# Performance work log

Measured on AMD Instinct MI355X. Metric: run time of the kernel, lower is better.

Reference implementation:

```python
import jax, jax.numpy as jnp
import numpy as np

S, B, I, H, MLP, K = 1024, 64, 512, 256, 512, 64  # seq_len, batch, input, hidden, mlp, n_sections


def setup_inputs() -> dict:
    key = jax.random.key(0)
    ks = jax.random.split(key, 12)
    inputs = jax.random.normal(ks[0], (S, B, I), jnp.float32)
    input_length = jnp.full((B,), S, dtype=jnp.int32)  # full-length seqs -> pack/pad is identity
    # contiguous section boundaries per document; indices address pad_output of length S+1
    bounds = jnp.sort(jax.random.randint(ks[1], (B, K + 1), 0, S + 1), axis=1)
    begin = bounds[:, :-1].astype(jnp.int32)
    end = bounds[:, 1:].astype(jnp.int32)
    # one-hot section membership per token: [B, S, K]
    sec = jax.random.randint(ks[2], (B, S), 0, K)
    section_indicator = jax.nn.one_hot(sec, K, dtype=jnp.float32)
    s = 1.0 / np.sqrt(H)
    u = lambda k, shape: jax.random.uniform(k, shape, jnp.float32, -s, s)
    params = {
        'W_ih_f': u(ks[3], (3 * H, I)), 'W_hh_f': u(ks[4], (3 * H, H)),
        'b_ih_f': u(ks[5], (3 * H,)), 'b_hh_f': u(ks[5], (3 * H,)),
        'W_ih_b': u(ks[6], (3 * H, I)), 'W_hh_b': u(ks[7], (3 * H, H)),
        'b_ih_b': u(ks[8], (3 * H,)), 'b_hh_b': u(ks[8], (3 * H,)),
        'W1': u(ks[9], (MLP, 4 * H)), 'b1': u(ks[9], (MLP,)),
        'W2': u(ks[10], (1, MLP)), 'b2': u(ks[10], (1,)),
    }
    return dict(inputs=inputs, input_length=input_length,
                section_indicator=section_indicator, begin=begin, end=end, **params)


def _gru_dir(x, Wi, Wh, bi, bh, reverse):
    """One direction of a torch-style GRU. x: [S,B,I] -> hiddens [S,B,H]."""
    xi = jnp.einsum('sbi,gi->sbg', x, Wi) + bi  # precompute input projections [S,B,3H]
    Bsz = x.shape[1]
    Hn = Wh.shape[1]

    def step(h, xt):
        gh = h @ Wh.T + bh
        xr, xz, xn = jnp.split(xt, 3, axis=-1)
        hr, hz, hn = jnp.split(gh, 3, axis=-1)
        r = jax.nn.sigmoid(xr + hr)
        z = jax.nn.sigmoid(xz + hz)
        n = jnp.tanh(xn + r * hn)
        hnew = (1.0 - z) * n + z * h
        return hnew, hnew

    h0 = jnp.zeros((Bsz, Hn), x.dtype)
    _, hs = jax.lax.scan(step, h0, xi, reverse=reverse)
    return hs


def reference(inputs, input_length, section_indicator, begin, end,
              W_ih_f, W_hh_f, b_ih_f, b_hh_f,
              W_ih_b, W_hh_b, b_ih_b, b_hh_b,
              W1, b1, W2, b2):
    # bi-GRU (dropout layers are identity in eval mode)
    out_f = _gru_dir(inputs, W_ih_f, W_hh_f, b_ih_f, b_hh_f, reverse=False)
    out_b = _gru_dir(inputs, W_ih_b, W_hh_b, b_ih_b, b_hh_b, reverse=True)
    output = jnp.concatenate([out_f, out_b], axis=-1)  # [S,B,2H]
    # prepend zero row along time: pad_output [S+1,B,2H]
    pad_output = jnp.concatenate([jnp.zeros((1,) + output.shape[1:], output.dtype), output], axis=0)
    po = jnp.transpose(pad_output, (1, 0, 2))  # [B,S+1,2H]
    g_end = jnp.take_along_axis(po, end[:, :, None], axis=1)    # [B,K,2H]
    g_beg = jnp.take_along_axis(po, begin[:, :, None], axis=1)  # [B,K,2H]
    Hn = output.shape[-1] // 2
    local = jnp.concatenate([g_end[..., :Hn] - g_beg[..., :Hn],
                             g_beg[..., Hn:] - g_end[..., Hn:]], axis=-1)  # [B,K,2H]
    lcr = jnp.einsum('bsk,bkd->bsd', section_indicator, local)  # [B,S,2H]
    lcr = jnp.transpose(lcr, (1, 0, 2))  # [S,B,2H]
    mlp_in = jnp.concatenate([output, lcr], axis=-1)  # [S,B,4H]
    h1 = jax.nn.relu(mlp_in @ W1.T + b1)
    out = h1 @ W2.T + b2  # [S,B,1]
    return out
```

## Files before the change

### kernel.cpp

```cpp
#include <hip/hip_runtime.h>

typedef unsigned short u16;
typedef __attribute__((ext_vector_type(2))) unsigned short u16x2;
typedef __attribute__((ext_vector_type(8))) short short8;
typedef __attribute__((ext_vector_type(4))) float f32x4;
typedef __attribute__((ext_vector_type(4))) int i32x4;

#define T_CHUNK 128
#define XI_DIRSZ ((size_t)T_CHUNK * 49152)

__device__ __forceinline__ u16 f2bf(float f) {
  unsigned u = __float_as_uint(f);
  u += 0x7FFFu + ((u >> 16) & 1u);
  return (u16)(u >> 16);
}
__device__ __forceinline__ float bf2f(u16 v) { return __uint_as_float(((unsigned)v) << 16); }
__device__ __forceinline__ short8 cvt8(const float* __restrict__ p) {
  float4 a = ((const float4*)p)[0];
  float4 b = ((const float4*)p)[1];
  short8 r;
  r[0] = (short)f2bf(a.x); r[1] = (short)f2bf(a.y); r[2] = (short)f2bf(a.z); r[3] = (short)f2bf(a.w);
  r[4] = (short)f2bf(b.x); r[5] = (short)f2bf(b.y); r[6] = (short)f2bf(b.z); r[7] = (short)f2bf(b.w);
  return r;
}

__global__ __launch_bounds__(256) void k_diag(float* o, float v) {
  if (threadIdx.x == 0 && blockIdx.x == 0) o[0] = v;
}

__global__ __launch_bounds__(256) void k_cvt(const float* __restrict__ s, u16* __restrict__ d, int n) {
  int i = blockIdx.x * 256 + threadIdx.x;
  int st = gridDim.x * 256;
  for (; i < n; i += st) d[i] = f2bf(s[i]);
}

__global__ __launch_bounds__(64) void k_quantw(const float* __restrict__ Wf, const float* __restrict__ Wb,
                                               signed char* __restrict__ Wq, float* __restrict__ rscale) {
  const int row = blockIdx.x;
  const int l = threadIdx.x;
  const float* src = (row < 768) ? (Wf + (size_t)row * 256) : (Wb + (size_t)(row - 768) * 256);
  float4 v = ((const float4*)src)[l];
  float m = fmaxf(fmaxf(fabsf(v.x), fabsf(v.y)), fmaxf(fabsf(v.z), fabsf(v.w)));
#pragma unroll
  for (int off = 32; off; off >>= 1) m = fmaxf(m, __shfl_xor(m, off));
  const float s = 127.f / m;
  char4 q;
  q.x = (signed char)(int)__builtin_rintf(v.x * s);
  q.y = (signed char)(int)__builtin_rintf(v.y * s);
  q.z = (signed char)(int)__builtin_rintf(v.z * s);
  q.w = (signed char)(int)__builtin_rintf(v.w * s);
  ((char4*)(Wq + (size_t)row * 256))[l] = q;
  if (l == 0) rscale[row] = m / (127.f * 127.f);
}

__device__ __forceinline__ int swz8b(int row, int off) {
  return row * 256 + ((((off >> 4) ^ (row * 5)) & 15) << 4) + (off & 15);
}

__device__ __forceinline__ void proj_body(int pid, int cn, const float* __restrict__ x,
                                          const u16* __restrict__ WihB, const float* __restrict__ bihf,
                                          const float* __restrict__ bihb, u16* __restrict__ xi,
                                          u16* Al, u16* Bl) {
  const int tid = threadIdx.x;
  const int l = tid & 63, w = tid >> 6;
  const int lm = l & 15, lq = l >> 4;
  const int dir = pid >= 1536;
  const int q = dir ? pid - 1536 : pid;
  const int r8 = q & 7, rest = q >> 3;
  const int bx = rest % 12;
  const int by = (rest / 12) * 8 + r8;
  const float* A = x + ((size_t)(dir ? (1024 - (cn + 1) * T_CHUNK) : (cn * T_CHUNK)) + by) * 32768;
  const u16* Bw = WihB + (size_t)dir * 393216;
  const float* bias = dir ? bihb : bihf;
  u16* xo = xi + ((size_t)((cn & 1) * 2 + dir)) * XI_DIRSZ;

  const int n0 = bx << 6;
  const int r0 = tid >> 3, c0 = (tid & 7) << 3;
  const int mt = w >> 1, nh = w & 1;
  f32x4 acc[2] = {};
  for (int k0 = 0; k0 < 512; k0 += 64) {
    __syncthreads();
    *(short8*)&Al[r0 * 72 + c0] = cvt8(A + (size_t)r0 * 512 + k0 + c0);
    *(short8*)&Bl[r0 * 72 + c0] = *(const short8*)(Bw + (size_t)(n0 + r0) * 512 + k0 + c0);
    __syncthreads();
#pragma unroll
    for (int kk = 0; kk < 2; ++kk) {
      short8 af = *(const short8*)&Al[(mt * 16 + lm) * 72 + kk * 32 + lq * 8];
#pragma unroll
      for (int ntp = 0; ntp < 2; ++ntp) {
        short8 bf = *(const short8*)&Bl[((nh * 2 + ntp) * 16 + lm) * 72 + kk * 32 + lq * 8];
        acc[ntp] = __builtin_amdgcn_mfma_f32_16x16x32_bf16(af, bf, acc[ntp], 0, 0, 0);
      }
    }
  }
#pragma unroll
  for (int ntp = 0; ntp < 2; ++ntp) {
    int n = n0 + (nh * 2 + ntp) * 16 + lm;
    float bv = bias[n];
#pragma unroll
    for (int r = 0; r < 4; ++r) {
      int b = mt * 16 + lq * 4 + r;
      xo[(((size_t)by * 8 + (b >> 3)) * 768 + n) * 8 + (b & 7)] = f2bf(acc[ntp][r] + bv);
    }
  }
}

__global__ __launch_bounds__(512, 2) void k_proj0(const float* __restrict__ x, const u16* __restrict__ WihB,
                                                  const float* __restrict__ bihf, const float* __restrict__ bihb,
                                                  u16* __restrict__ xi) {
  __shared__ __align__(16) u16 Al[64 * 72];
  __shared__ __align__(16) u16 Bl[64 * 72];
  proj_body(blockIdx.x, 0, x, WihB, bihf, bihb, xi, Al, Bl);
}

__global__ __launch_bounds__(512, 1) void k_fused(
    const float* __restrict__ x, const u16* __restrict__ WihB,
    const float* __restrict__ bihf, const float* __restrict__ bihb,
    u16* __restrict__ xi, const signed char* __restrict__ Wq, const float* __restrict__ rscale,
    const float* __restrict__ bhhf, const float* __restrict__ bhhb,
    float* __restrict__ carry, u16* __restrict__ ob, int chunk, int nscan) {
  __shared__ __align__(16) signed char hb8[2][1024];
  __shared__ __align__(16) u16 Al[64 * 72];
  __shared__ __align__(16) u16 Bl[64 * 72];

  const int tid = threadIdx.x;
  const int l = tid & 63, w = tid >> 6;
  const int lm = l & 15, lq = l >> 4;

  if ((int)blockIdx.x >= nscan) {
    proj_body(blockIdx.x - nscan, chunk + 1, x, WihB, bihf, bihb, xi, Al, Bl);
    return;
  }

  __builtin_amdgcn_s_setprio(1);
  const int dir = blockIdx.x >> 4;
  const int grp = blockIdx.x & 15;
  const int jhL = lq >> 1;
  const int b0 = (lq & 1) << 1;
  const int jL = w * 32 + jhL * 16 + lm;
  const int arow = lm & 3;
  const float* bhh = dir ? bhhb : bhhf;
  const u16* xic = xi + ((size_t)((chunk & 1) * 2 + dir)) * XI_DIRSZ;

  i32x4 bw[6][4];
#pragma unroll
  for (int g = 0; g < 3; ++g)
#pragma unroll
    for (int jh = 0; jh < 2; ++jh) {
      const int row = dir * 768 + g * 256 + w * 32 + jh * 16 + lm;
      const signed char* rp = Wq + (size_t)row * 256 + lq * 16;
#pragma unroll
      for (int kk = 0; kk < 4; ++kk) bw[g * 2 + jh][kk] = *(const i32x4*)(rp + kk * 64);
    }
  float rs[3];
#pragma unroll
  for (int g = 0; g < 3; ++g) rs[g] = rscale[dir * 768 + g * 256 + jL];
  const float bR = bhh[jL], bZ = bhh[256 + jL], bN = bhh[512 + jL];

  signed char* hbb = &hb8[0][0];
  float hreg[2];
  if (chunk == 0) {
    hreg[0] = 0.f; hreg[1] = 0.f;
    if (tid < 512) ((unsigned*)hbb)[tid] = 0;
  } else {
#pragma unroll
    for (int i = 0; i < 2; ++i) {
      float v = carry[(size_t)(dir * 64 + grp * 4 + b0 + i) * 256 + jL];
      hreg[i] = v;
      hbb[swz8b(b0 + i, jL)] = (signed char)(int)__builtin_rintf(fminf(fmaxf(v, -1.f), 1.f) * 127.f);
    }
  }

  const int stL0 = dir ? (T_CHUNK - 1) : 0;
  const u16* p_xi = xic + ((size_t)stL0 * 8 + (grp >> 1)) * 6144 + (size_t)jL * 8 + (grp & 1) * 4 + b0;
  const int tg0 = dir ? (1023 - chunk * T_CHUNK) : (chunk * T_CHUNK);
  u16* p_ob = ob + ((size_t)(tg0 * 64 + grp * 4 + b0)) * 512 + dir * 256 + jL;
  const ptrdiff_t dxi = dir ? -49152 : 49152;
  const ptrdiff_t dob = dir ? -32768 : 32768;
  __syncthreads();

  u16x2 xv[3];
#pragma unroll
  for (int g = 0; g < 3; ++g) xv[g] = *(const u16x2*)(p_xi + g * 2048);

  for (int st = 0; st < T_CHUNK; ++st) {
    const int cur = st & 1;
    const signed char* hcur = hbb + cur * 1024;
    i32x4 a4[4];
#pragma unroll
    for (int kk = 0; kk < 4; ++kk) a4[kk] = *(const i32x4*)(hcur + swz8b(arow, kk * 64 + lq * 16));
    p_xi += dxi;
    u16x2 xn[3];
    if (st < T_CHUNK - 1) {
#pragma unroll
      for (int g = 0; g < 3; ++g) xn[g] = *(const u16x2*)(p_xi + g * 2048);
    }

    i32x4 acc[2][3] = {};
#pragma unroll
    for (int kk = 0; kk < 4; ++kk)
#pragma unroll
      for (int jh = 0; jh < 2; ++jh)
#pragma unroll
        for (int g = 0; g < 3; ++g)
          acc[jh][g] = __builtin_amdgcn_mfma_i32_16x16x64_i8(a4[kk], bw[g * 2 + jh][kk], acc[jh][g], 0, 0, 0);

    signed char* hnxt = hbb + (cur ^ 1) * 1024;
    i32x4 accS[3];
#pragma unroll
    for (int g = 0; g < 3; ++g) accS[g] = (lq >= 2) ? acc[1][g] : acc[0][g];
#pragma unroll
    for (int i = 0; i < 2; ++i) {
      float fr = (float)((lq & 1) ? accS[0][2 + i] : accS[0][i]) * rs[0];
      float fz = (float)((lq & 1) ? accS[1][2 + i] : accS[1][i]) * rs[1];
      float fn = (float)((lq & 1) ? accS[2][2 + i] : accS[2][i]) * rs[2];
      float ar = bf2f(xv[0][i]) + fr + bR;
      float az = bf2f(xv[1][i]) + fz + bZ;
      float rr = __builtin_amdgcn_rcpf(1.f + __expf(-ar));
      float zz = __builtin_amdgcn_rcpf(1.f + __expf(-az));
      float an = bf2f(xv[2][i]) + rr * (fn + bN);
      float nn = 2.f * __builtin_amdgcn_rcpf(1.f + __expf(-2.f * an)) - 1.f;
      float hv = nn + zz * (hreg[i] - nn);
      hreg[i] = hv;
      hnxt[swz8b(b0 + i, jL)] = (signed char)(int)__builtin_rintf(fminf(fmaxf(hv, -1.f), 1.f) * 127.f);
      p_ob[(size_t)i * 512] = f2bf(hv);
    }
#pragma unroll
    for (int g = 0; g < 3; ++g) xv[g] = xn[g];
    p_ob += dob;
    asm volatile("s_waitcnt lgkmcnt(0)\n\ts_barrier" ::: "memory");
  }
  __builtin_amdgcn_s_setprio(0);
#pragma unroll
  for (int i = 0; i < 2; ++i)
    carry[(size_t)(dir * 64 + grp * 4 + b0 + i) * 256 + jL] = hreg[i];
}

__global__ __launch_bounds__(256) void k_local(const u16* __restrict__ ob, const int* __restrict__ bg,
                                               const int* __restrict__ en, u16* __restrict__ loc) {
  const int b = blockIdx.y, k = blockIdx.x, j = threadIdx.x;
  const int e = en[b * 64 + k], g = bg[b * 64 + k];
  const float ef  = e ? bf2f(ob[(size_t)((e - 1) * 64 + b) * 512 + j]) : 0.f;
  const float bf_ = g ? bf2f(ob[(size_t)((g - 1) * 64 + b) * 512 + j]) : 0.f;
  const float eb  = e ? bf2f(ob[(size_t)((e - 1) * 64 + b) * 512 + 256 + j]) : 0.f;
  const float bb_ = g ? bf2f(ob[(size_t)((g - 1) * 64 + b) * 512 + 256 + j]) : 0.f;
  const size_t o = ((size_t)b * 64 + k) * 512;
  loc[o + j] = f2bf(ef - bf_);
  loc[o + 256 + j] = f2bf(bb_ - eb);
}

__global__ __launch_bounds__(256) void k_sec(const float* __restrict__ ind, int* __restrict__ sec) {
  const int idx = blockIdx.x * 256 + threadIdx.x;
  const int s = idx >> 6, b = idx & 63;
  const float* row = ind + ((size_t)b * 1024 + s) * 64;
  int kk = 0;
  for (int q = 0; q < 64; ++q)
    if (row[q] > 0.5f) kk = q;
  sec[idx] = kk;
}

__global__ __launch_bounds__(256) void k_gemm_mlp(const u16* __restrict__ obb, const u16* __restrict__ locb,
                                                  const int* __restrict__ sec, const u16* __restrict__ W1b,
                                                  const float* __restrict__ b1, const float* __restrict__ W2,
                                                  float* __restrict__ partial) {
  __shared__ __align__(16) u16 Bl[128][64];
  const int tid = threadIdx.x;
  const int l = tid & 63, w = tid >> 6;
  const int lm = l & 15, lq = l >> 4;
  const int bid = blockIdx.x;
  const int mb = (bid >> 5) * 8 + (bid & 7);
  const int nh = (bid >> 3) & 3;
  const int m0 = mb << 7, n0 = nh << 7;

  const u16* pa[2];
  const u16* la[2];
#pragma unroll
  for (int mt = 0; mt < 2; ++mt) {
    int mA = m0 + w * 32 + mt * 16 + lm;
    pa[mt] = obb + (size_t)mA * 512;
    la[mt] = locb + ((size_t)(mA & 63) * 64 + sec[mA]) * 512 - 512;
  }
  const int br = tid >> 1;
  const int bh = tid & 1;
  const u16* wrow = W1b + (size_t)(n0 + br) * 1024 + bh * 32;

  short8 rb[4];
#pragma unroll
  for (int c = 0; c < 4; ++c) rb[c] = *(const short8*)(wrow + c * 8);
  short8 rA[2][2];
#pragma unroll
  for (int mt = 0; mt < 2; ++mt)
#pragma unroll
    for (int kk = 0; kk < 2; ++kk) rA[mt][kk] = *(const short8*)(pa[mt] + kk * 32 + lq * 8);

  f32x4 acc[2][8] = {};
  for (int k0 = 0; k0 < 1024; k0 += 64) {
    __syncthreads();
#pragma unroll
    for (int c = 0; c < 4; ++c)
      *(short8*)&Bl[br][(((bh * 4 + c) ^ (br & 7)) << 3)] = rb[c];
    __syncthreads();
    short8 aCur[2][2];
#pragma unroll
    for (int mt = 0; mt < 2; ++mt)
#pragma unroll
      for (int kk = 0; kk < 2; ++kk) aCur[mt][kk] = rA[mt][kk];
    if (k0 < 960) {
      const int kn = k0 + 64;
#pragma unroll
      for (int c = 0; c < 4; ++c) rb[c] = *(const short8*)(wrow + kn + c * 8);
#pragma unroll
      for (int mt = 0; mt < 2; ++mt) {
        const u16* base = (kn < 512) ? pa[mt] : la[mt];
#pragma unroll
        for (int kk = 0; kk < 2; ++kk) rA[mt][kk] = *(const short8*)(base + kn + kk * 32 + lq * 8);
      }
    }
#pragma unroll
    for (int kk = 0; kk < 2; ++kk)
#pragma unroll
      for (int nt = 0; nt < 8; ++nt) {
        const int rrow = nt * 16 + lm;
        short8 bf = *(const short8*)&Bl[rrow][(((kk * 4 + lq) ^ (rrow & 7)) << 3)];
#pragma unroll
        for (int mt = 0; mt < 2; ++mt)
          acc[mt][nt] = __builtin_amdgcn_mfma_f32_16x16x32_bf16(aCur[mt][kk], bf, acc[mt][nt], 0, 0, 0);
      }
  }
  float s[2][4];
#pragma unroll
  for (int mt = 0; mt < 2; ++mt)
#pragma unroll
    for (int r = 0; r < 4; ++r) s[mt][r] = 0.f;
#pragma unroll
  for (int nt = 0; nt < 8; ++nt) {
    int n = n0 + nt * 16 + lm;
    float bb = b1[n], ww = W2[n];
#pragma unroll
    for (int mt = 0; mt < 2; ++mt)
#pragma unroll
      for (int r = 0; r < 4; ++r) s[mt][r] += fmaxf(acc[mt][nt][r] + bb, 0.f) * ww;
  }
#pragma unroll
  for (int off = 1; off < 16; off <<= 1)
#pragma unroll
    for (int mt = 0; mt < 2; ++mt)
#pragma unroll
      for (int r = 0; r < 4; ++r) s[mt][r] += __shfl_xor(s[mt][r], off);
  if (lm == 0) {
#pragma unroll
    for (int mt = 0; mt < 2; ++mt)
#pragma unroll
      for (int r = 0; r < 4; ++r)
        partial[(size_t)nh * 65536 + m0 + w * 32 + mt * 16 + lq * 4 + r] = s[mt][r];
  }
}

__global__ __launch_bounds__(256) void k_fin2(const float* __restrict__ partial, const float* __restrict__ b2,
                                              float* __restrict__ o) {
  const int i = blockIdx.x * 256 + threadIdx.x;
  float s = b2[0];
#pragma unroll
  for (int q = 0; q < 4; ++q) s += partial[(size_t)q * 65536 + i];
  o[i] = s;
}

extern "C" void kernel_launch(void* const* d_in, const int* in_sizes, int n_in,
                              void* d_out, int out_size, void* d_ws, size_t ws_size,
                              hipStream_t stream) {
  (void)in_sizes; (void)n_in; (void)out_size;
  const float* x    = (const float*)d_in[0];
  const float* sind = (const float*)d_in[2];
  const int*   beg  = (const int*)d_in[3];
  const int*   endi = (const int*)d_in[4];
  const float* Wihf = (const float*)d_in[5];
  const float* Whhf = (const float*)d_in[6];
  const float* bihf = (const float*)d_in[7];
  const float* bhhf = (const float*)d_in[8];
  const float* Wihb = (const float*)d_in[9];
  const float* Whhb = (const float*)d_in[10];
  const float* bihb = (const float*)d_in[11];
  const float* bhhb = (const float*)d_in[12];
  const float* W1   = (const float*)d_in[13];
  const float* b1   = (const float*)d_in[14];
  const float* W2   = (const float*)d_in[15];
  const float* b2   = (const float*)d_in[16];

  const size_t NEED = 124911616ull;
  if (ws_size < NEED) {
    k_diag<<<dim3(1), dim3(256), 0, stream>>>((float*)d_out, 1000.f + (float)(ws_size >> 20));
    return;
  }

  char* ws = (char*)d_ws;
  u16*   xibuf = (u16*)(ws);
  u16*   obb   = (u16*)(ws + 50331648);
  u16*   locb  = (u16*)(ws + 117440512);
  int*   sec   = (int*)(ws + 121634816);
  float* part  = (float*)(ws + 121896960);
  u16*   W1b   = (u16*)(ws + 122945536);
  signed char* Wq = (signed char*)(ws + 123994112);
  float* rscale = (float*)(ws + 124387328);
  float* carry = (float*)(ws + 124780544);
  u16*   WihB  = (u16*)(ws + 117440512);

  k_quantw<<<dim3(1536), dim3(64), 0, stream>>>(Whhf, Whhb, Wq, rscale);
  k_cvt<<<dim3(128), dim3(256), 0, stream>>>(Wihf, WihB, 393216);
  k_cvt<<<dim3(128), dim3(256), 0, stream>>>(Wihb, WihB + 393216, 393216);
  k_cvt<<<dim3(256), dim3(256), 0, stream>>>(W1, W1b, 524288);
  k_sec<<<dim3(256), dim3(256), 0, stream>>>(sind, sec);

  k_proj0<<<dim3(3072), dim3(512), 0, stream>>>(x, WihB, bihf, bihb, xibuf);
  for (int c = 0; c < 8; ++c)
    k_fused<<<dim3(c < 7 ? 3104 : 32), dim3(512), 65536, stream>>>(x, WihB, bihf, bihb, xibuf, Wq, rscale,
                                                                   bhhf, bhhb, carry, obb, c, 32);

  k_local<<<dim3(64, 64), dim3(256), 0, stream>>>(obb, beg, endi, locb);
  k_gemm_mlp<<<dim3(2048), dim3(256), 0, stream>>>(obb, locb, sec, W1b, b1, W2, part);
  k_fin2<<<dim3(256), dim3(256), 0, stream>>>(part, b2, (float*)d_out);
}
```

Baseline: 979.9 us.

## Split GRU scan across 64 blocks with two batch rows each

New measurement: 1.011 ms. 1.03x slower.

```diff
diff --git a/kernel.cpp b/kernel.cpp
--- a/kernel.cpp
+++ b/kernel.cpp
@@ -1,7 +1,6 @@
 #include <hip/hip_runtime.h>
 
 typedef unsigned short u16;
-typedef __attribute__((ext_vector_type(2))) unsigned short u16x2;
 typedef __attribute__((ext_vector_type(8))) short short8;
 typedef __attribute__((ext_vector_type(4))) float f32x4;
 typedef __attribute__((ext_vector_type(4))) int i32x4;
@@ -53,7 +52,7 @@
   if (l == 0) rscale[row] = m / (127.f * 127.f);
 }
 
-__device__ __forceinline__ int swz8b(int row, int off) {
+__device__ __forceinline__ int swz2(int row, int off) {
   return row * 256 + ((((off >> 4) ^ (row * 5)) & 15) << 4) + (off & 15);
 }
 
@@ -113,13 +112,13 @@
   proj_body(blockIdx.x, 0, x, WihB, bihf, bihb, xi, Al, Bl);
 }
 
-__global__ __launch_bounds__(512, 1) void k_fused(
+__global__ __launch_bounds__(512, 2) void k_fused(
     const float* __restrict__ x, const u16* __restrict__ WihB,
     const float* __restrict__ bihf, const float* __restrict__ bihb,
     u16* __restrict__ xi, const signed char* __restrict__ Wq, const float* __restrict__ rscale,
     const float* __restrict__ bhhf, const float* __restrict__ bhhb,
     float* __restrict__ carry, u16* __restrict__ ob, int chunk, int nscan) {
-  __shared__ __align__(16) signed char hb8[2][1024];
+  __shared__ __align__(16) signed char hb8[2][512];
   __shared__ __align__(16) u16 Al[64 * 72];
   __shared__ __align__(16) u16 Bl[64 * 72];
 
@@ -133,12 +132,12 @@
   }
 
   __builtin_amdgcn_s_setprio(1);
-  const int dir = blockIdx.x >> 4;
-  const int grp = blockIdx.x & 15;
+  const int dir = blockIdx.x >> 5;
+  const int grp = blockIdx.x & 31;
   const int jhL = lq >> 1;
-  const int b0 = (lq & 1) << 1;
+  const int bL = lq & 1;
   const int jL = w * 32 + jhL * 16 + lm;
-  const int arow = lm & 3;
+  const int arow = lm & 1;
   const float* bhh = dir ? bhhb : bhhf;
   const u16* xic = xi + ((size_t)((chunk & 1) * 2 + dir)) * XI_DIRSZ;
 
@@ -158,42 +157,39 @@
   const float bR = bhh[jL], bZ = bhh[256 + jL], bN = bhh[512 + jL];
 
   signed char* hbb = &hb8[0][0];
-  float hreg[2];
+  float hreg;
   if (chunk == 0) {
-    hreg[0] = 0.f; hreg[1] = 0.f;
-    if (tid < 512) ((unsigned*)hbb)[tid] = 0;
+    hreg = 0.f;
+    if (tid < 256) ((unsigned*)hbb)[tid] = 0;
   } else {
-#pragma unroll
-    for (int i = 0; i < 2; ++i) {
-      float v = carry[(size_t)(dir * 64 + grp * 4 + b0 + i) * 256 + jL];
-      hreg[i] = v;
-      hbb[swz8b(b0 + i, jL)] = (signed char)(int)__builtin_rintf(fminf(fmaxf(v, -1.f), 1.f) * 127.f);
-    }
+    float v = carry[(size_t)(dir * 64 + grp * 2 + bL) * 256 + jL];
+    hreg = v;
+    hbb[swz2(bL, jL)] = (signed char)(int)__builtin_rintf(fminf(fmaxf(v, -1.f), 1.f) * 127.f);
   }
 
   const int stL0 = dir ? (T_CHUNK - 1) : 0;
-  const u16* p_xi = xic + ((size_t)stL0 * 8 + (grp >> 1)) * 6144 + (size_t)jL * 8 + (grp & 1) * 4 + b0;
+  const u16* p_xi = xic + ((size_t)stL0 * 8 + (grp >> 2)) * 6144 + (size_t)jL * 8 + (grp & 3) * 2 + bL;
   const int tg0 = dir ? (1023 - chunk * T_CHUNK) : (chunk * T_CHUNK);
-  u16* p_ob = ob + ((size_t)(tg0 * 64 + grp * 4 + b0)) * 512 + dir * 256 + jL;
+  u16* p_ob = ob + ((size_t)(tg0 * 64 + grp * 2 + bL)) * 512 + dir * 256 + jL;
   const ptrdiff_t dxi = dir ? -49152 : 49152;
   const ptrdiff_t dob = dir ? -32768 : 32768;
   __syncthreads();
 
-  u16x2 xv[3];
-#pragma unroll
-  for (int g = 0; g < 3; ++g) xv[g] = *(const u16x2*)(p_xi + g * 2048);
+  u16 xv[3];
+#pragma unroll
+  for (int g = 0; g < 3; ++g) xv[g] = p_xi[g * 2048];
 
   for (int st = 0; st < T_CHUNK; ++st) {
     const int cur = st & 1;
-    const signed char* hcur = hbb + cur * 1024;
+    const signed char* hcur = hbb + cur * 512;
     i32x4 a4[4];
 #pragma unroll
-    for (int kk = 0; kk < 4; ++kk) a4[kk] = *(const i32x4*)(hcur + swz8b(arow, kk * 64 + lq * 16));
+    for (int kk = 0; kk < 4; ++kk) a4[kk] = *(const i32x4*)(hcur + swz2(arow, kk * 64 + lq * 16));
     p_xi += dxi;
-    u16x2 xn[3];
+    u16 xn[3];
     if (st < T_CHUNK - 1) {
 #pragma unroll
-      for (int g = 0; g < 3; ++g) xn[g] = *(const u16x2*)(p_xi + g * 2048);
+      for (int g = 0; g < 3; ++g) xn[g] = p_xi[g * 2048];
     }
 
     i32x4 acc[2][3] = {};
@@ -205,25 +201,24 @@
         for (int g = 0; g < 3; ++g)
           acc[jh][g] = __builtin_amdgcn_mfma_i32_16x16x64_i8(a4[kk], bw[g * 2 + jh][kk], acc[jh][g], 0, 0, 0);
 
-    signed char* hnxt = hbb + (cur ^ 1) * 1024;
-    i32x4 accS[3];
-#pragma unroll
-    for (int g = 0; g < 3; ++g) accS[g] = (lq >= 2) ? acc[1][g] : acc[0][g];
-#pragma unroll
-    for (int i = 0; i < 2; ++i) {
-      float fr = (float)((lq & 1) ? accS[0][2 + i] : accS[0][i]) * rs[0];
-      float fz = (float)((lq & 1) ? accS[1][2 + i] : accS[1][i]) * rs[1];
-      float fn = (float)((lq & 1) ? accS[2][2 + i] : accS[2][i]) * rs[2];
-      float ar = bf2f(xv[0][i]) + fr + bR;
-      float az = bf2f(xv[1][i]) + fz + bZ;
+    signed char* hnxt = hbb + (cur ^ 1) * 512;
+    {
+      int vrI = (jhL ? acc[1][0][bL] : acc[0][0][bL]);
+      int vzI = (jhL ? acc[1][1][bL] : acc[0][1][bL]);
+      int vnI = (jhL ? acc[1][2][bL] : acc[0][2][bL]);
+      float fr = (float)vrI * rs[0];
+      float fz = (float)vzI * rs[1];
+      float fn = (float)vnI * rs[2];
+      float ar = bf2f(xv[0]) + fr + bR;
+      float az = bf2f(xv[1]) + fz + bZ;
       float rr = __builtin_amdgcn_rcpf(1.f + __expf(-ar));
       float zz = __builtin_amdgcn_rcpf(1.f + __expf(-az));
-      float an = bf2f(xv[2][i]) + rr * (fn + bN);
+      float an = bf2f(xv[2]) + rr * (fn + bN);
       float nn = 2.f * __builtin_amdgcn_rcpf(1.f + __expf(-2.f * an)) - 1.f;
-      float hv = nn + zz * (hreg[i] - nn);
-      hreg[i] = hv;
-      hnxt[swz8b(b0 + i, jL)] = (signed char)(int)__builtin_rintf(fminf(fmaxf(hv, -1.f), 1.f) * 127.f);
-      p_ob[(size_t)i * 512] = f2bf(hv);
+      float hv = nn + zz * (hreg - nn);
+      hreg = hv;
+      hnxt[swz2(bL, jL)] = (signed char)(int)__builtin_rintf(fminf(fmaxf(hv, -1.f), 1.f) * 127.f);
+      p_ob[0] = f2bf(hv);
     }
 #pragma unroll
     for (int g = 0; g < 3; ++g) xv[g] = xn[g];
@@ -231,9 +226,7 @@
     asm volatile("s_waitcnt lgkmcnt(0)\n\ts_barrier" ::: "memory");
   }
   __builtin_amdgcn_s_setprio(0);
-#pragma unroll
-  for (int i = 0; i < 2; ++i)
-    carry[(size_t)(dir * 64 + grp * 4 + b0 + i) * 256 + jL] = hreg[i];
+  carry[(size_t)(dir * 64 + grp * 2 + bL) * 256 + jL] = hreg;
 }
 
 __global__ __launch_bounds__(256) void k_local(const u16* __restrict__ ob, const int* __restrict__ bg,
@@ -412,8 +405,8 @@
 
   k_proj0<<<dim3(3072), dim3(512), 0, stream>>>(x, WihB, bihf, bihb, xibuf);
   for (int c = 0; c < 8; ++c)
-    k_fused<<<dim3(c < 7 ? 3104 : 32), dim3(512), 65536, stream>>>(x, WihB, bihf, bihb, xibuf, Wq, rscale,
-                                                                   bhhf, bhhb, carry, obb, c, 32);
+    k_fused<<<dim3(c < 7 ? 3136 : 64), dim3(512), 0, stream>>>(x, WihB, bihf, bihb, xibuf, Wq, rscale,
+                                                               bhhf, bhhb, carry, obb, c, 64);
 
   k_local<<<dim3(64, 64), dim3(256), 0, stream>>>(obb, beg, endi, locb);
   k_gemm_mlp<<<dim3(2048), dim3(256), 0, stream>>>(obb, locb, sec, W1b, b1, W2, part);
```
